# Kernel optimization log

Hardware: AMD Instinct MI355X
Metric: run time of the kernel (lower is better)

Reference implementation:

```python
import jax, jax.numpy as jnp
import numpy as np

B = 8192; N_LEAF = 34; N_SUB = 11; D0 = 32; ES = 64; EA = 128; H = 4
ETH = slice(0, 8); IP = slice(8, 19); TCP = slice(19, 34)
TCPF = slice(0, 8); IPF = slice(8, 11)


def setup_inputs() -> dict:
    key = jax.random.key(0)
    ks = jax.random.split(key, 32)
    w = lambda i, s: jax.random.normal(ks[i], s, dtype=jnp.float32) * 0.05
    return {
        "leaf_feats": jax.random.normal(ks[0], (B, N_LEAF, D0), dtype=jnp.float32),
        "sub_feats": jax.random.normal(ks[1], (B, N_SUB, D0), dtype=jnp.float32),
        "sub_align_W": w(2, (N_SUB, D0, ES)), "sub_align_b": w(3, (N_SUB, ES)),
        "leaf_align_W": w(4, (N_LEAF, D0, EA)), "leaf_align_b": w(5, (N_LEAF, EA)),
        "parent_align_W": w(6, (2, ES, EA)), "parent_align_b": w(7, (2, EA)),
        "sA_cls": w(8, (2, ES)), "sA_Wqkv": w(9, (2, 3 * ES, ES)), "sA_bqkv": w(10, (2, 3 * ES)),
        "sA_Wo": w(11, (2, ES, ES)), "sA_bo": w(12, (2, ES)),
        "sA_lng": jnp.ones((2, ES), jnp.float32), "sA_lnb": jnp.zeros((2, ES), jnp.float32),
        "sA_W1": w(13, (2, ES, 4 * ES)), "sA_b1": w(14, (2, 4 * ES)),
        "sA_W2": w(15, (2, 4 * ES, ES)), "sA_b2": w(16, (2, ES)),
        "pA_cls": w(17, (4, EA)), "pA_Wqkv": w(18, (4, 3 * EA, EA)), "pA_bqkv": w(19, (4, 3 * EA)),
        "pA_Wo": w(20, (4, EA, EA)), "pA_bo": w(21, (4, EA)),
        "pA_lng": jnp.ones((4, EA), jnp.float32), "pA_lnb": jnp.zeros((4, EA), jnp.float32),
        "pA_W1": w(22, (4, EA, 4 * EA)), "pA_b1": w(23, (4, 4 * EA)),
        "pA_W2": w(24, (4, 4 * EA, EA)), "pA_b2": w(25, (4, EA)),
        "clf_W": w(26, (EA, 2)), "clf_b": w(27, (2,)),
    }


def _ln(t, g, b):
    m = jnp.mean(t, -1, keepdims=True)
    v = jnp.var(t, -1, keepdims=True)
    return (t - m) / jnp.sqrt(v + 1e-5) * g + b


def _agg(x, cls, Wqkv, bqkv, Wo, bo, lng, lnb, W1, b1, W2, b2):
    # AttentionAggregator: prepend CLS, MHA, shared LayerNorm twice, FFN; return CLS output.
    Bx, _, E = x.shape
    d = E // H
    xc = jnp.concatenate([jnp.broadcast_to(cls, (Bx, 1, E)), x], axis=1)  # [B,S,E]
    S = xc.shape[1]
    qkv = xc @ Wqkv.T + bqkv                      # torch MHA in_proj layout [3E,E]
    q, k, v = jnp.split(qkv, 3, axis=-1)
    sh = lambda t: t.reshape(Bx, S, H, d).transpose(0, 2, 1, 3)
    q, k, v = sh(q), sh(k), sh(v)
    a = jax.nn.softmax(jnp.einsum('bhqd,bhkd->bhqk', q, k) * (1.0 / np.sqrt(d)), axis=-1)
    o = jnp.einsum('bhqk,bhkd->bhqd', a, v).transpose(0, 2, 1, 3).reshape(Bx, S, E)
    o = o @ Wo.T + bo
    h = _ln(xc + o, lng, lnb)
    f = jax.nn.gelu(h @ W1 + b1, approximate=False) @ W2 + b2
    h = _ln(h + f, lng, lnb)
    return h[:, 0]


def reference(leaf_feats, sub_feats, sub_align_W, sub_align_b, leaf_align_W, leaf_align_b,
              parent_align_W, parent_align_b,
              sA_cls, sA_Wqkv, sA_bqkv, sA_Wo, sA_bo, sA_lng, sA_lnb, sA_W1, sA_b1, sA_W2, sA_b2,
              pA_cls, pA_Wqkv, pA_bqkv, pA_Wo, pA_bo, pA_lng, pA_lnb, pA_W1, pA_b1, pA_W2, pA_b2,
              clf_W, clf_b):
    sA = lambda i: (sA_cls[i], sA_Wqkv[i], sA_bqkv[i], sA_Wo[i], sA_bo[i], sA_lng[i], sA_lnb[i],
                    sA_W1[i], sA_b1[i], sA_W2[i], sA_b2[i])
    pA = lambda i: (pA_cls[i], pA_Wqkv[i], pA_bqkv[i], pA_Wo[i], pA_bo[i], pA_lng[i], pA_lnb[i],
                    pA_W1[i], pA_b1[i], pA_W2[i], pA_b2[i])
    # subfield align (per-subfield Linear, batched) + aggregate
    sub_al = jnp.einsum('bsd,sde->bse', sub_feats, sub_align_W) + sub_align_b  # [B,11,64]
    tcpf = _agg(sub_al[:, TCPF], *sA(0))   # tcp.flags -> [B,64]
    ipf = _agg(sub_al[:, IPF], *sA(1))     # ip.flags  -> [B,64]
    # per-field aligners to aligned_dim=128
    leaf_al = jnp.einsum('bfd,fde->bfe', leaf_feats, leaf_align_W) + leaf_align_b  # [B,34,128]
    parent_al = jnp.stack([tcpf @ parent_align_W[0] + parent_align_b[0],
                           ipf @ parent_align_W[1] + parent_align_b[1]], axis=1)   # [B,2,128]
    eth_vec = _agg(leaf_al[:, ETH], *pA(0))
    ip_vec = _agg(jnp.concatenate([leaf_al[:, IP], parent_al[:, 1:2]], axis=1), *pA(1))
    tcp_vec = _agg(jnp.concatenate([leaf_al[:, TCP], parent_al[:, 0:1]], axis=1), *pA(2))
    pkt = _agg(jnp.stack([eth_vec, ip_vec, tcp_vec], axis=1), *pA(3))
    return pkt @ clf_W + clf_b
```

## Files before the change

kernel.cpp:

```cpp
#include <hip/hip_runtime.h>
#include <math.h>

#define G 4
#define NT 256


enum {
  I_LEAF = 0, I_SUB, I_SAW, I_SAB, I_LAW, I_LAB, I_PAW, I_PAB,
  I_SCLS, I_SWQKV, I_SBQKV, I_SWO, I_SBO, I_SLNG, I_SLNB, I_SW1, I_SB1, I_SW2, I_SB2,
  I_PCLS, I_PWQKV, I_PBQKV, I_PWO, I_PBO, I_PLNG, I_PLNB, I_PW1, I_PB1, I_PW2, I_PB2,
  I_CLFW, I_CLFB
};

struct P {
  const float* in[32];
  float* parent_al;
  float* vecs;
  float* out;
};

__device__ float g_usb[6][520];

__device__ __align__(16) float g_svT[2][64 * 64];
__device__ __align__(16) float g_soT[2][64 * 64];
__device__ __align__(16) float g_pvT[4][128 * 128];
__device__ __align__(16) float g_poT[4][128 * 128];

__device__ __forceinline__ void LD8(const float* p, float* o) {
  float4 a = ((const float4*)p)[0], b = ((const float4*)p)[1];
  o[0] = a.x; o[1] = a.y; o[2] = a.z; o[3] = a.w;
  o[4] = b.x; o[5] = b.y; o[6] = b.z; o[7] = b.w;
}
__device__ __forceinline__ void fma8(float& acc, const float* x, const float* w) {
#pragma unroll
  for (int i = 0; i < 8; ++i) acc += x[i] * w[i];
}
__device__ __forceinline__ float gelu(float v) {
  return 0.5f * v * (1.0f + erff(v * 0.70710678118654752f));
}

template <int E>
__device__ void ln_rows(float* buf, const float* __restrict__ gg, const float* __restrict__ bb) {
  const int w = threadIdx.x >> 6, lane = threadIdx.x & 63;
  for (int g = w; g < G; g += 4) {
    float* row = buf + g * E;
    float s = 0.f, s2 = 0.f;
    for (int e = lane; e < E; e += 64) { float x = row[e]; s += x; s2 += x * x; }
#pragma unroll
    for (int off = 1; off < 64; off <<= 1) {
      s += __shfl_xor(s, off, 64);
      s2 += __shfl_xor(s2, off, 64);
    }
    float m = s / (float)E;
    float inv = 1.0f / sqrtf(s2 / (float)E - m * m + 1e-5f);
    for (int e = lane; e < E; e += 64) row[e] = (row[e] - m) * inv * gg[e] + bb[e];
  }
}

__global__ __launch_bounds__(NT) void k_setup(P p) {
  const int a = blockIdx.x;
  const int tid = threadIdx.x;
  __shared__ float clsb[128];
  __shared__ float qb[128];
  int E;
  const float *Wq, *bq, *cls;
  if (a < 2) {
    E = 64;
    Wq = p.in[I_SWQKV] + (size_t)a * 192 * 64;
    bq = p.in[I_SBQKV] + a * 192;
    cls = p.in[I_SCLS] + a * 64;
  } else {
    E = 128;
    int i = a - 2;
    Wq = p.in[I_PWQKV] + (size_t)i * 384 * 128;
    bq = p.in[I_PBQKV] + i * 384;
    cls = p.in[I_PCLS] + i * 128;
  }
  const int D = E / 4;
  const float scale = (E == 64) ? 0.25f : 0.17677669529663687f;
  if (tid < E) clsb[tid] = cls[tid];
  __syncthreads();
  if (tid < E) {
    float acc = bq[tid];
    const float* w = Wq + (size_t)tid * E;
    for (int k = 0; k < E; k += 8) {
      float wv[8];
      LD8(w + k, wv);
#pragma unroll
      for (int ii = 0; ii < 8; ++ii) acc += clsb[k + ii] * wv[ii];
    }
    qb[tid] = acc;
  }
  __syncthreads();
  if (tid < E) {
    for (int h = 0; h < 4; ++h) {
      float acc = 0.f;
      for (int d = 0; d < D; ++d)
        acc += Wq[(size_t)(E + h * D + d) * E + tid] * qb[h * D + d];
      g_usb[a][h * E + tid] = acc * scale;
    }
  }
  if (tid < 4) {
    float acc = 0.f;
    for (int d = 0; d < D; ++d) acc += qb[tid * D + d] * bq[E + tid * D + d];
    g_usb[a][4 * E + tid] = acc * scale;
  }
  if (a < 2) {
    const float* Wv = p.in[I_SWQKV] + (size_t)a * 192 * 64 + 2 * 64 * 64;
    const float* Wo = p.in[I_SWO] + (size_t)a * 64 * 64;
    for (int idx = tid; idx < 64 * 64; idx += NT) {
      int k = idx >> 6, e = idx & 63;
      g_svT[a][idx] = Wv[(size_t)e * 64 + k];
      g_soT[a][idx] = Wo[(size_t)e * 64 + k];
    }
  } else {
    int i = a - 2;
    const float* Wv = p.in[I_PWQKV] + (size_t)i * 384 * 128 + 2 * 128 * 128;
    const float* Wo = p.in[I_PWO] + (size_t)i * 128 * 128;
    for (int idx = tid; idx < 128 * 128; idx += NT) {
      int k = idx >> 7, e = idx & 127;
      g_pvT[i][idx] = Wv[(size_t)e * 128 + k];
      g_poT[i][idx] = Wo[(size_t)e * 128 + k];
    }
  }
}

template <int E, int T, int XP>
__device__ void agg_run(const float* X, const float* clsb,
                        const float* uL, const float* sbL,
                        const float* __restrict__ WvT, const float* __restrict__ bv,
                        const float* __restrict__ WoT, const float* __restrict__ bo,
                        const float* __restrict__ lng, const float* __restrict__ lnb,
                        const float* __restrict__ W1, const float* __restrict__ b1,
                        const float* __restrict__ W2, const float* __restrict__ b2,
                        float* att, float* xbar, float* ob, float* hb, float* mid,
                        float* partial) {
  const int tid = threadIdx.x;
  constexpr int S = T + 1, KS = NT / E, KCH = E / KS;
  constexpr int M1 = (4 * E) / NT, KCH2 = (4 * E) / KS;

  for (int i = tid; i < G * 4 * S; i += NT) {
    int s = i % S, hh = (i / S) % 4, g = i / (4 * S);
    const float* u = uL + hh * XP;
    const float* x = (s == 0) ? clsb : (X + (size_t)(g * T + s - 1) * XP);
    float acc = sbL[hh];
    for (int k = 0; k < E; k += 8) {
      float xv[8], uv[8];
      LD8(x + k, xv);
      LD8(u + k, uv);
      fma8(acc, xv, uv);
    }
    att[(g * 4 + hh) * S + s] = acc;
  }
  __syncthreads();
  for (int i = tid; i < G * 4; i += NT) {
    float* a = att + i * S;
    float mx = a[0];
    for (int s = 1; s < S; ++s) mx = fmaxf(mx, a[s]);
    float sum = 0.f;
    for (int s = 0; s < S; ++s) { float e = expf(a[s] - mx); a[s] = e; sum += e; }
    float inv = 1.0f / sum;
    for (int s = 0; s < S; ++s) a[s] *= inv;
  }
  __syncthreads();
  constexpr int NI = (G * 4 * E) / NT;
  float xacc[NI];
#pragma unroll
  for (int n = 0; n < NI; ++n) {
    int i = tid + n * NT;
    int k = i % E, hh = (i / E) % 4, g = i / (4 * E);
    const float* a = att + (g * 4 + hh) * S;
    float acc = a[0] * clsb[k];
    for (int s = 1; s < S; ++s) acc += a[s] * X[(size_t)(g * T + s - 1) * XP + k];
    xacc[n] = acc;
  }
  __syncthreads();
#pragma unroll
  for (int n = 0; n < NI; ++n) xbar[tid + n * NT] = xacc[n];
  __syncthreads();
  {
    const int e = tid % E, ks = tid / E, hh = e / (E / 4);
    float acc[G];
#pragma unroll
    for (int g = 0; g < G; ++g) acc[g] = 0.f;
    for (int kc = 0; kc < KCH; kc += 8) {
      float wv[8];
#pragma unroll
      for (int ii = 0; ii < 8; ++ii)
        wv[ii] = WvT[(size_t)(ks * KCH + kc + ii) * E + e];
#pragma unroll
      for (int g = 0; g < G; ++g) {
        float xv[8];
        LD8(xbar + (g * 4 + hh) * E + ks * KCH + kc, xv);
        fma8(acc[g], xv, wv);
      }
    }
#pragma unroll
    for (int g = 0; g < G; ++g) partial[(ks * G + g) * E + e] = acc[g];
  }
  __syncthreads();
  for (int i = tid; i < G * E; i += NT) {
    int e = i % E, g = i / E;
    float v = bv[e];
#pragma unroll
    for (int ks = 0; ks < KS; ++ks) v += partial[(ks * G + g) * E + e];
    ob[g * E + e] = v;
  }
  __syncthreads();
  {
    const int e = tid % E, ks = tid / E;
    float acc[G];
#pragma unroll
    for (int g = 0; g < G; ++g) acc[g] = 0.f;
    for (int kc = 0; kc < KCH; kc += 8) {
      float wv[8];
#pragma unroll
      for (int ii = 0; ii < 8; ++ii)
        wv[ii] = WoT[(size_t)(ks * KCH + kc + ii) * E + e];
#pragma unroll
      for (int g = 0; g < G; ++g) {
        float xv[8];
        LD8(ob + g * E + ks * KCH + kc, xv);
        fma8(acc[g], xv, wv);
      }
    }
#pragma unroll
    for (int g = 0; g < G; ++g) partial[(ks * G + g) * E + e] = acc[g];
  }
  __syncthreads();
  for (int i = tid; i < G * E; i += NT) {
    int e = i % E, g = i / E;
    float v = bo[e] + clsb[e];
#pragma unroll
    for (int ks = 0; ks < KS; ++ks) v += partial[(ks * G + g) * E + e];
    hb[g * E + e] = v;
  }
  __syncthreads();
  ln_rows<E>(hb, lng, lnb);
  __syncthreads();
  {
    float acc[M1][G];
#pragma unroll
    for (int r = 0; r < M1; ++r)
#pragma unroll
      for (int g = 0; g < G; ++g) acc[r][g] = 0.f;
    for (int j = 0; j < E; j += 8) {
      float wv[M1][8];
#pragma unroll
      for (int ii = 0; ii < 8; ++ii) {
        if constexpr (M1 == 2) {
          float2 w2 = *(const float2*)(W1 + (size_t)(j + ii) * 4 * E + 2 * tid);
          wv[0][ii] = w2.x;
          wv[1][ii] = w2.y;
        } else {
          wv[0][ii] = W1[(size_t)(j + ii) * 4 * E + tid];
        }
      }
#pragma unroll
      for (int g = 0; g < G; ++g) {
        float xv[8];
        LD8(hb + g * E + j, xv);
#pragma unroll
        for (int r = 0; r < M1; ++r) fma8(acc[r][g], xv, wv[r]);
      }
    }
#pragma unroll
    for (int r = 0; r < M1; ++r) {
      int m = tid * M1 + r;
      float bias = b1[m];
#pragma unroll
      for (int g = 0; g < G; ++g) mid[g * 4 * E + m] = gelu(acc[r][g] + bias);
    }
  }
  __syncthreads();
  {
    const int e = tid % E, ks = tid / E, m0 = ks * KCH2;
    float acc[G];
#pragma unroll
    for (int g = 0; g < G; ++g) acc[g] = 0.f;
    for (int mc = 0; mc < KCH2; mc += 8) {
      float wv[8];
#pragma unroll
      for (int ii = 0; ii < 8; ++ii) wv[ii] = W2[(size_t)(m0 + mc + ii) * E + e];
#pragma unroll
      for (int g = 0; g < G; ++g) {
        float xv[8];
        LD8(mid + g * 4 * E + m0 + mc, xv);
        fma8(acc[g], xv, wv);
      }
    }
#pragma unroll
    for (int g = 0; g < G; ++g) partial[(ks * G + g) * E + e] = acc[g];
  }
  __syncthreads();
  for (int i = tid; i < G * E; i += NT) {
    int e = i % E, g = i / E;
    float v = b2[e] + hb[g * E + e];
#pragma unroll
    for (int ks = 0; ks < KS; ++ks) v += partial[(ks * G + g) * E + e];
    ob[g * E + e] = v;
  }
  __syncthreads();
  ln_rows<E>(ob, lng, lnb);
  __syncthreads();
}

template <int T, int F0, int AI>
__device__ void sub_body(const P& p, int b0) {
  constexpr int XP = 68;
  const int tid = threadIdx.x;
  __shared__ __align__(16) float X[G * T * XP];
  __shared__ __align__(16) float clsb[64];
  __shared__ __align__(16) float uL[4 * XP];
  __shared__ __align__(16) float sbL[4];
  __shared__ __align__(16) float att[G * 4 * (T + 1)];
  __shared__ __align__(16) float xbar[G * 4 * 64];
  __shared__ __align__(16) float ob[G * 64];
  __shared__ __align__(16) float hb[G * 64];
  __shared__ __align__(16) float mid[G * 256];
  __shared__ __align__(16) float partial[4 * G * 64];

  const float* subf = p.in[I_SUB];
  const float* saW = p.in[I_SAW];
  const float* sab = p.in[I_SAB];
  for (int i = tid; i < T * 64; i += NT) {
    int f = i / 64, e = i % 64;
    float bias = sab[(F0 + f) * 64 + e];
    float acc[G];
#pragma unroll
    for (int g = 0; g < G; ++g) acc[g] = bias;
    for (int d = 0; d < 32; d += 8) {
      float wv[8];
#pragma unroll
      for (int ii = 0; ii < 8; ++ii)
        wv[ii] = saW[(size_t)((F0 + f) * 32 + d + ii) * 64 + e];
#pragma unroll
      for (int g = 0; g < G; ++g) {
        float xv[8];
        LD8(subf + (size_t)(b0 + g) * 352 + (F0 + f) * 32 + d, xv);
        fma8(acc[g], xv, wv);
      }
    }
#pragma unroll
    for (int g = 0; g < G; ++g) X[(g * T + f) * XP + e] = acc[g];
  }
  for (int i = tid; i < 4 * 64; i += NT) uL[(i >> 6) * XP + (i & 63)] = g_usb[AI][i];
  if (tid < 4) sbL[tid] = g_usb[AI][256 + tid];
  if (tid < 64) clsb[tid] = p.in[I_SCLS][AI * 64 + tid];
  __syncthreads();

  agg_run<64, T, XP>(X, clsb, uL, sbL,
                     g_svT[AI], p.in[I_SBQKV] + AI * 192 + 128,
                     g_soT[AI], p.in[I_SBO] + AI * 64,
                     p.in[I_SLNG] + AI * 64, p.in[I_SLNB] + AI * 64,
                     p.in[I_SW1] + AI * 64 * 256, p.in[I_SB1] + AI * 256,
                     p.in[I_SW2] + AI * 256 * 64, p.in[I_SB2] + AI * 64,
                     att, xbar, ob, hb, mid, partial);
  for (int i = tid; i < G * 64; i += NT) {
    int e = i % 64, g = i / 64;
    p.vecs[(size_t)(b0 + g) * 384 + AI * 64 + e] = ob[g * 64 + e];
  }
}

__global__ __launch_bounds__(NT, 4) void k_sub_agg0(P p) { sub_body<8, 0, 0>(p, blockIdx.x * G); }
__global__ __launch_bounds__(NT, 4) void k_sub_agg1(P p) { sub_body<3, 8, 1>(p, blockIdx.x * G); }

__global__ __launch_bounds__(NT, 4) void k_pal(P p) {
  __shared__ __align__(16) float tf[G * 128];
  const int tid = threadIdx.x, b0 = blockIdx.x * G;
  for (int i = tid; i < G * 128; i += NT) {
    int g = i / 128, r = i % 128;
    tf[i] = p.vecs[(size_t)(b0 + g) * 384 + r];
  }
  __syncthreads();
  const int pi = tid >> 7, e = tid & 127;
  const float* paW = p.in[I_PAW];
  float bias = p.in[I_PAB][pi * 128 + e];
  float acc[G];
#pragma unroll
  for (int g = 0; g < G; ++g) acc[g] = bias;
  for (int j = 0; j < 64; j += 8) {
    float wv[8];
#pragma unroll
    for (int ii = 0; ii < 8; ++ii) wv[ii] = paW[(size_t)(pi * 64 + j + ii) * 128 + e];
#pragma unroll
    for (int g = 0; g < G; ++g) {
      float xv[8];
      LD8(tf + g * 128 + pi * 64 + j, xv);
      fma8(acc[g], xv, wv);
    }
  }
#pragma unroll
  for (int g = 0; g < G; ++g)
    p.parent_al[(size_t)(b0 + g) * 256 + pi * 128 + e] = acc[g];
}

#define PXP 132
#define OVL 6144

template <int T, int F, int F0, int PAR, int AI>
__device__ void parent_body(const P& p, int b0, float* arena, float* clsb,
                            float* uL, float* sbL, float* att) {
  const int tid = threadIdx.x;
  float* X = arena;
  const float* leaf = p.in[I_LEAF];
  const float* laW = p.in[I_LAW];
  const float* lab = p.in[I_LAB];
  for (int i = tid; i < F * 128; i += NT) {
    int f = i / 128, e = i % 128;
    float bias = lab[(F0 + f) * 128 + e];
    float acc[G];
#pragma unroll
    for (int g = 0; g < G; ++g) acc[g] = bias;
    for (int d = 0; d < 32; d += 8) {
      float wv[8];
#pragma unroll
      for (int ii = 0; ii < 8; ++ii)
        wv[ii] = laW[(size_t)((F0 + f) * 32 + d + ii) * 128 + e];
#pragma unroll
      for (int g = 0; g < G; ++g) {
        float xv[8];
        LD8(leaf + (size_t)(b0 + g) * 1088 + (F0 + f) * 32 + d, xv);
        fma8(acc[g], xv, wv);
      }
    }
#pragma unroll
    for (int g = 0; g < G; ++g) X[(g * T + f) * PXP + e] = acc[g];
  }
  if constexpr (PAR >= 0) {
    for (int i = tid; i < G * 128; i += NT) {
      int g = i / 128, e = i % 128;
      X[(g * T + T - 1) * PXP + e] = p.parent_al[(size_t)(b0 + g) * 256 + PAR * 128 + e];
    }
  }
  for (int i = tid; i < 4 * 128; i += NT) uL[(i >> 7) * PXP + (i & 127)] = g_usb[2 + AI][i];
  if (tid < 4) sbL[tid] = g_usb[2 + AI][512 + tid];
  if (tid < 128) clsb[tid] = p.in[I_PCLS][AI * 128 + tid];
  __syncthreads();

  float* xbar = arena;
  float* partial = arena + 2048;
  float* ob = arena + 3072;
  float* hb = arena + 3584;
  float* mid = arena + 4096;
  agg_run<128, T, PXP>(X, clsb, uL, sbL,
                       g_pvT[AI], p.in[I_PBQKV] + AI * 384 + 256,
                       g_poT[AI], p.in[I_PBO] + AI * 128,
                       p.in[I_PLNG] + AI * 128, p.in[I_PLNB] + AI * 128,
                       p.in[I_PW1] + (size_t)AI * 128 * 512, p.in[I_PB1] + AI * 512,
                       p.in[I_PW2] + (size_t)AI * 512 * 128, p.in[I_PB2] + AI * 128,
                       att, xbar, ob, hb, mid, partial);
  for (int i = tid; i < G * 128; i += NT) {
    int e = i % 128, g = i / 128;
    p.vecs[(size_t)(b0 + g) * 384 + AI * 128 + e] = ob[g * 128 + e];
  }
}

#define PARENT_KERNEL(NAME, T, F, F0, PAR, AI, ASZ)                         \
__global__ __launch_bounds__(NT, 4) void NAME(P p) {                        \
  __shared__ __align__(16) float arena[ASZ];                                \
  __shared__ __align__(16) float clsb[128];                                 \
  __shared__ __align__(16) float uL[4 * PXP];                               \
  __shared__ __align__(16) float sbL[4];                                    \
  __shared__ __align__(16) float att[G * 4 * (T + 1)];                      \
  parent_body<T, F, F0, PAR, AI>(p, blockIdx.x * G, arena, clsb, uL, sbL, att); \
}

PARENT_KERNEL(k_parent0,  8,  8,  0, -1, 0, OVL)
PARENT_KERNEL(k_parent1, 12, 11,  8,  1, 1, G * 12 * PXP)
PARENT_KERNEL(k_parent2, 16, 15, 19,  0, 2, G * 16 * PXP)

__global__ __launch_bounds__(NT, 4) void k_pkt(P p) {
  __shared__ __align__(16) float arena[OVL];
  __shared__ __align__(16) float clsb[128];
  __shared__ __align__(16) float uL[4 * PXP];
  __shared__ __align__(16) float sbL[4];
  __shared__ __align__(16) float att[G * 4 * 4];
  const int tid = threadIdx.x, b0 = blockIdx.x * G;
  float* X = arena;

  for (int i = tid; i < 3 * G * 128; i += NT) {
    int e = i % 128, g = (i / 128) % G, t = i / (G * 128);
    X[(g * 3 + t) * PXP + e] = p.vecs[(size_t)(b0 + g) * 384 + t * 128 + e];
  }
  for (int i = tid; i < 4 * 128; i += NT) uL[(i >> 7) * PXP + (i & 127)] = g_usb[5][i];
  if (tid < 4) sbL[tid] = g_usb[5][512 + tid];
  if (tid < 128) clsb[tid] = p.in[I_PCLS][3 * 128 + tid];
  __syncthreads();

  float* xbar = arena;
  float* partial = arena + 2048;
  float* ob = arena + 3072;
  float* hb = arena + 3584;
  float* mid = arena + 4096;
  agg_run<128, 3, PXP>(X, clsb, uL, sbL,
                       g_pvT[3], p.in[I_PBQKV] + 3 * 384 + 256,
                       g_poT[3], p.in[I_PBO] + 3 * 128,
                       p.in[I_PLNG] + 3 * 128, p.in[I_PLNB] + 3 * 128,
                       p.in[I_PW1] + (size_t)3 * 128 * 512, p.in[I_PB1] + 3 * 512,
                       p.in[I_PW2] + (size_t)3 * 512 * 128, p.in[I_PB2] + 3 * 128,
                       att, xbar, ob, hb, mid, partial);

  if (tid < G * 2) {
    int g = tid >> 1, c = tid & 1;
    const float* cw = p.in[I_CLFW];
    float acc = p.in[I_CLFB][c];
    for (int j = 0; j < 128; ++j) acc += ob[g * 128 + j] * cw[j * 2 + c];
    p.out[(size_t)(b0 + g) * 2 + c] = acc;
  }
}

extern "C" void kernel_launch(void* const* d_in, const int* in_sizes, int n_in,
                              void* d_out, int out_size, void* d_ws, size_t ws_size,
                              hipStream_t stream) {
  P p;
  for (int i = 0; i < 32; ++i) p.in[i] = (const float*)d_in[i];
  const int B = in_sizes[0] / (34 * 32);
  float* ws = (float*)d_ws;
  p.parent_al = ws;
  p.vecs = ws + (size_t)B * 256;
  p.out = (float*)d_out;

  k_setup<<<dim3(6), dim3(NT), 0, stream>>>(p);
  k_sub_agg0<<<dim3(B / G), dim3(NT), 0, stream>>>(p);
  k_sub_agg1<<<dim3(B / G), dim3(NT), 0, stream>>>(p);
  k_pal<<<dim3(B / G), dim3(NT), 0, stream>>>(p);
  k_parent0<<<dim3(B / G), dim3(NT), 0, stream>>>(p);
  k_parent1<<<dim3(B / G), dim3(NT), 0, stream>>>(p);
  k_parent2<<<dim3(B / G), dim3(NT), 0, stream>>>(p);
  k_pkt<<<dim3(B / G), dim3(NT), 0, stream>>>(p);
}
```

Before: 943.1 us.

## Split each aggregator kernel into separate attention and FFN kernels

Each attention aggregator kernel is split in two. The first computes attention plus the first LayerNorm and writes the intermediate to global workspace. The second reloads it and runs the FFN and second LayerNorm. The aim is to shrink per-kernel shared memory and register footprint so more blocks fit per CU. The cost is six more kernel launches plus an extra global write and read of the intermediate vectors, and the FFN kernels may become weight-bandwidth bound.

```diff
diff --git a/kernel.cpp b/kernel.cpp
--- a/kernel.cpp
+++ b/kernel.cpp
@@ -126,18 +126,15 @@
 }
 
 template <int E, int T, int XP>
-__device__ void agg_run(const float* X, const float* clsb,
-                        const float* uL, const float* sbL,
-                        const float* __restrict__ WvT, const float* __restrict__ bv,
-                        const float* __restrict__ WoT, const float* __restrict__ bo,
-                        const float* __restrict__ lng, const float* __restrict__ lnb,
-                        const float* __restrict__ W1, const float* __restrict__ b1,
-                        const float* __restrict__ W2, const float* __restrict__ b2,
-                        float* att, float* xbar, float* ob, float* hb, float* mid,
-                        float* partial) {
+__device__ void agg_attn(const float* X, const float* clsb,
+                         const float* uL, const float* sbL,
+                         const float* __restrict__ WvT, const float* __restrict__ bv,
+                         const float* __restrict__ WoT, const float* __restrict__ bo,
+                         const float* __restrict__ lng, const float* __restrict__ lnb,
+                         float* att, float* xbar, float* ob, float* hb,
+                         float* partial) {
   const int tid = threadIdx.x;
   constexpr int S = T + 1, KS = NT / E, KCH = E / KS;
-  constexpr int M1 = (4 * E) / NT, KCH2 = (4 * E) / KS;
 
   for (int i = tid; i < G * 4 * S; i += NT) {
     int s = i % S, hh = (i / S) % 4, g = i / (4 * S);
@@ -238,6 +235,15 @@
   __syncthreads();
   ln_rows<E>(hb, lng, lnb);
   __syncthreads();
+}
+
+template <int E>
+__device__ void agg_ffn(const float* __restrict__ W1, const float* __restrict__ b1,
+                        const float* __restrict__ W2, const float* __restrict__ b2,
+                        const float* __restrict__ lng, const float* __restrict__ lnb,
+                        float* hb, float* mid, float* partial, float* ob) {
+  const int tid = threadIdx.x;
+  constexpr int KS = NT / E, M1 = (4 * E) / NT, KCH2 = (4 * E) / KS;
   {
     float acc[M1][G];
 #pragma unroll
@@ -305,20 +311,16 @@
   __syncthreads();
 }
 
-template <int T, int F0, int AI>
-__device__ void sub_body(const P& p, int b0) {
+template <int T, int F0, int AI, int ASZ>
+__device__ void sub_attn_body(const P& p, int b0) {
   constexpr int XP = 68;
   const int tid = threadIdx.x;
-  __shared__ __align__(16) float X[G * T * XP];
+  __shared__ __align__(16) float arena[ASZ];
   __shared__ __align__(16) float clsb[64];
   __shared__ __align__(16) float uL[4 * XP];
   __shared__ __align__(16) float sbL[4];
   __shared__ __align__(16) float att[G * 4 * (T + 1)];
-  __shared__ __align__(16) float xbar[G * 4 * 64];
-  __shared__ __align__(16) float ob[G * 64];
-  __shared__ __align__(16) float hb[G * 64];
-  __shared__ __align__(16) float mid[G * 256];
-  __shared__ __align__(16) float partial[4 * G * 64];
+  float* X = arena;
 
   const float* subf = p.in[I_SUB];
   const float* saW = p.in[I_SAW];
@@ -349,21 +351,47 @@
   if (tid < 64) clsb[tid] = p.in[I_SCLS][AI * 64 + tid];
   __syncthreads();
 
-  agg_run<64, T, XP>(X, clsb, uL, sbL,
-                     g_svT[AI], p.in[I_SBQKV] + AI * 192 + 128,
-                     g_soT[AI], p.in[I_SBO] + AI * 64,
-                     p.in[I_SLNG] + AI * 64, p.in[I_SLNB] + AI * 64,
-                     p.in[I_SW1] + AI * 64 * 256, p.in[I_SB1] + AI * 256,
-                     p.in[I_SW2] + AI * 256 * 64, p.in[I_SB2] + AI * 64,
-                     att, xbar, ob, hb, mid, partial);
+  float* xbar = arena;
+  float* partial = arena + 1024;
+  float* ob = arena + 2048;
+  float* hb = arena + 2304;
+  agg_attn<64, T, XP>(X, clsb, uL, sbL,
+                      g_svT[AI], p.in[I_SBQKV] + AI * 192 + 128,
+                      g_soT[AI], p.in[I_SBO] + AI * 64,
+                      p.in[I_SLNG] + AI * 64, p.in[I_SLNB] + AI * 64,
+                      att, xbar, ob, hb, partial);
+  for (int i = tid; i < G * 64; i += NT) {
+    int e = i % 64, g = i / 64;
+    p.vecs[(size_t)(b0 + g) * 384 + AI * 64 + e] = hb[g * 64 + e];
+  }
+}
+
+__global__ __launch_bounds__(NT, 4) void k_sattn0(P p) { sub_attn_body<8, 0, 0, 2560>(p, blockIdx.x * G); }
+__global__ __launch_bounds__(NT, 4) void k_sattn1(P p) { sub_attn_body<3, 8, 1, 2560>(p, blockIdx.x * G); }
+
+template <int AI>
+__device__ void sub_ffn_body(const P& p, int b0) {
+  const int tid = threadIdx.x;
+  __shared__ __align__(16) float hb[G * 64];
+  __shared__ __align__(16) float mid[G * 256];
+  __shared__ __align__(16) float partial[4 * G * 64];
+  __shared__ __align__(16) float ob[G * 64];
+  for (int i = tid; i < G * 64; i += NT) {
+    int e = i % 64, g = i / 64;
+    hb[i] = p.vecs[(size_t)(b0 + g) * 384 + AI * 64 + e];
+  }
+  __syncthreads();
+  agg_ffn<64>(p.in[I_SW1] + AI * 64 * 256, p.in[I_SB1] + AI * 256,
+              p.in[I_SW2] + AI * 256 * 64, p.in[I_SB2] + AI * 64,
+              p.in[I_SLNG] + AI * 64, p.in[I_SLNB] + AI * 64,
+              hb, mid, partial, ob);
   for (int i = tid; i < G * 64; i += NT) {
     int e = i % 64, g = i / 64;
     p.vecs[(size_t)(b0 + g) * 384 + AI * 64 + e] = ob[g * 64 + e];
   }
 }
-
-__global__ __launch_bounds__(NT, 4) void k_sub_agg0(P p) { sub_body<8, 0, 0>(p, blockIdx.x * G); }
-__global__ __launch_bounds__(NT, 4) void k_sub_agg1(P p) { sub_body<3, 8, 1>(p, blockIdx.x * G); }
+__global__ __launch_bounds__(NT, 4) void k_sffn0(P p) { sub_ffn_body<0>(p, blockIdx.x * G); }
+__global__ __launch_bounds__(NT, 4) void k_sffn1(P p) { sub_ffn_body<1>(p, blockIdx.x * G); }
 
 __global__ __launch_bounds__(NT, 4) void k_pal(P p) {
   __shared__ __align__(16) float tf[G * 128];
@@ -396,11 +424,10 @@
 }
 
 #define PXP 132
-#define OVL 6144
 
 template <int T, int F, int F0, int PAR, int AI>
-__device__ void parent_body(const P& p, int b0, float* arena, float* clsb,
-                            float* uL, float* sbL, float* att) {
+__device__ void pattn_body(const P& p, int b0, float* arena, float* clsb,
+                           float* uL, float* sbL, float* att) {
   const int tid = threadIdx.x;
   float* X = arena;
   const float* leaf = p.in[I_LEAF];
@@ -442,36 +469,58 @@
   float* partial = arena + 2048;
   float* ob = arena + 3072;
   float* hb = arena + 3584;
-  float* mid = arena + 4096;
-  agg_run<128, T, PXP>(X, clsb, uL, sbL,
-                       g_pvT[AI], p.in[I_PBQKV] + AI * 384 + 256,
-                       g_poT[AI], p.in[I_PBO] + AI * 128,
-                       p.in[I_PLNG] + AI * 128, p.in[I_PLNB] + AI * 128,
-                       p.in[I_PW1] + (size_t)AI * 128 * 512, p.in[I_PB1] + AI * 512,
-                       p.in[I_PW2] + (size_t)AI * 512 * 128, p.in[I_PB2] + AI * 128,
-                       att, xbar, ob, hb, mid, partial);
+  agg_attn<128, T, PXP>(X, clsb, uL, sbL,
+                        g_pvT[AI], p.in[I_PBQKV] + AI * 384 + 256,
+                        g_poT[AI], p.in[I_PBO] + AI * 128,
+                        p.in[I_PLNG] + AI * 128, p.in[I_PLNB] + AI * 128,
+                        att, xbar, ob, hb, partial);
   for (int i = tid; i < G * 128; i += NT) {
     int e = i % 128, g = i / 128;
-    p.vecs[(size_t)(b0 + g) * 384 + AI * 128 + e] = ob[g * 128 + e];
-  }
-}
-
-#define PARENT_KERNEL(NAME, T, F, F0, PAR, AI, ASZ)                         \
+    p.vecs[(size_t)(b0 + g) * 384 + AI * 128 + e] = hb[g * 128 + e];
+  }
+}
+
+#define PATTN_KERNEL(NAME, T, F, F0, PAR, AI, ASZ)                          \
 __global__ __launch_bounds__(NT, 4) void NAME(P p) {                        \
   __shared__ __align__(16) float arena[ASZ];                                \
   __shared__ __align__(16) float clsb[128];                                 \
   __shared__ __align__(16) float uL[4 * PXP];                               \
   __shared__ __align__(16) float sbL[4];                                    \
   __shared__ __align__(16) float att[G * 4 * (T + 1)];                      \
-  parent_body<T, F, F0, PAR, AI>(p, blockIdx.x * G, arena, clsb, uL, sbL, att); \
-}
-
-PARENT_KERNEL(k_parent0,  8,  8,  0, -1, 0, OVL)
-PARENT_KERNEL(k_parent1, 12, 11,  8,  1, 1, G * 12 * PXP)
-PARENT_KERNEL(k_parent2, 16, 15, 19,  0, 2, G * 16 * PXP)
-
-__global__ __launch_bounds__(NT, 4) void k_pkt(P p) {
-  __shared__ __align__(16) float arena[OVL];
+  pattn_body<T, F, F0, PAR, AI>(p, blockIdx.x * G, arena, clsb, uL, sbL, att); \
+}
+
+PATTN_KERNEL(k_pattn0,  8,  8,  0, -1, 0, G * 8 * PXP)
+PATTN_KERNEL(k_pattn1, 12, 11,  8,  1, 1, G * 12 * PXP)
+PATTN_KERNEL(k_pattn2, 16, 15, 19,  0, 2, G * 16 * PXP)
+
+template <int AI>
+__device__ void pffn_body(const P& p, int b0) {
+  const int tid = threadIdx.x;
+  __shared__ __align__(16) float hb[G * 128];
+  __shared__ __align__(16) float mid[G * 512];
+  __shared__ __align__(16) float partial[2 * G * 128];
+  __shared__ __align__(16) float ob[G * 128];
+  for (int i = tid; i < G * 128; i += NT) {
+    int e = i % 128, g = i / 128;
+    hb[i] = p.vecs[(size_t)(b0 + g) * 384 + AI * 128 + e];
+  }
+  __syncthreads();
+  agg_ffn<128>(p.in[I_PW1] + (size_t)AI * 128 * 512, p.in[I_PB1] + AI * 512,
+               p.in[I_PW2] + (size_t)AI * 512 * 128, p.in[I_PB2] + AI * 128,
+               p.in[I_PLNG] + AI * 128, p.in[I_PLNB] + AI * 128,
+               hb, mid, partial, ob);
+  for (int i = tid; i < G * 128; i += NT) {
+    int e = i % 128, g = i / 128;
+    p.vecs[(size_t)(b0 + g) * 384 + AI * 128 + e] = ob[g * 128 + e];
+  }
+}
+__global__ __launch_bounds__(NT, 4) void k_pffn0(P p) { pffn_body<0>(p, blockIdx.x * G); }
+__global__ __launch_bounds__(NT, 4) void k_pffn1(P p) { pffn_body<1>(p, blockIdx.x * G); }
+__global__ __launch_bounds__(NT, 4) void k_pffn2(P p) { pffn_body<2>(p, blockIdx.x * G); }
+
+__global__ __launch_bounds__(NT, 4) void k_pkt_attn(P p) {
+  __shared__ __align__(16) float arena[4096];
   __shared__ __align__(16) float clsb[128];
   __shared__ __align__(16) float uL[4 * PXP];
   __shared__ __align__(16) float sbL[4];
@@ -492,15 +541,32 @@
   float* partial = arena + 2048;
   float* ob = arena + 3072;
   float* hb = arena + 3584;
-  float* mid = arena + 4096;
-  agg_run<128, 3, PXP>(X, clsb, uL, sbL,
-                       g_pvT[3], p.in[I_PBQKV] + 3 * 384 + 256,
-                       g_poT[3], p.in[I_PBO] + 3 * 128,
-                       p.in[I_PLNG] + 3 * 128, p.in[I_PLNB] + 3 * 128,
-                       p.in[I_PW1] + (size_t)3 * 128 * 512, p.in[I_PB1] + 3 * 512,
-                       p.in[I_PW2] + (size_t)3 * 512 * 128, p.in[I_PB2] + 3 * 128,
-                       att, xbar, ob, hb, mid, partial);
-
+  agg_attn<128, 3, PXP>(X, clsb, uL, sbL,
+                        g_pvT[3], p.in[I_PBQKV] + 3 * 384 + 256,
+                        g_poT[3], p.in[I_PBO] + 3 * 128,
+                        p.in[I_PLNG] + 3 * 128, p.in[I_PLNB] + 3 * 128,
+                        att, xbar, ob, hb, partial);
+  for (int i = tid; i < G * 128; i += NT) {
+    int e = i % 128, g = i / 128;
+    p.parent_al[(size_t)(b0 + g) * 256 + e] = hb[g * 128 + e];
+  }
+}
+
+__global__ __launch_bounds__(NT, 4) void k_pkt_ffn(P p) {
+  const int tid = threadIdx.x, b0 = blockIdx.x * G;
+  __shared__ __align__(16) float hb[G * 128];
+  __shared__ __align__(16) float mid[G * 512];
+  __shared__ __align__(16) float partial[2 * G * 128];
+  __shared__ __align__(16) float ob[G * 128];
+  for (int i = tid; i < G * 128; i += NT) {
+    int e = i % 128, g = i / 128;
+    hb[i] = p.parent_al[(size_t)(b0 + g) * 256 + e];
+  }
+  __syncthreads();
+  agg_ffn<128>(p.in[I_PW1] + (size_t)3 * 128 * 512, p.in[I_PB1] + 3 * 512,
+               p.in[I_PW2] + (size_t)3 * 512 * 128, p.in[I_PB2] + 3 * 128,
+               p.in[I_PLNG] + 3 * 128, p.in[I_PLNB] + 3 * 128,
+               hb, mid, partial, ob);
   if (tid < G * 2) {
     int g = tid >> 1, c = tid & 1;
     const float* cw = p.in[I_CLFW];
@@ -520,13 +586,20 @@
   p.parent_al = ws;
   p.vecs = ws + (size_t)B * 256;
   p.out = (float*)d_out;
-
-  k_setup<<<dim3(6), dim3(NT), 0, stream>>>(p);
-  k_sub_agg0<<<dim3(B / G), dim3(NT), 0, stream>>>(p);
-  k_sub_agg1<<<dim3(B / G), dim3(NT), 0, stream>>>(p);
-  k_pal<<<dim3(B / G), dim3(NT), 0, stream>>>(p);
-  k_parent0<<<dim3(B / G), dim3(NT), 0, stream>>>(p);
-  k_parent1<<<dim3(B / G), dim3(NT), 0, stream>>>(p);
-  k_parent2<<<dim3(B / G), dim3(NT), 0, stream>>>(p);
-  k_pkt<<<dim3(B / G), dim3(NT), 0, stream>>>(p);
-}
+  const dim3 grid(B / G), blk(NT);
+
+  k_setup<<<dim3(6), blk, 0, stream>>>(p);
+  k_sattn0<<<grid, blk, 0, stream>>>(p);
+  k_sffn0<<<grid, blk, 0, stream>>>(p);
+  k_sattn1<<<grid, blk, 0, stream>>>(p);
+  k_sffn1<<<grid, blk, 0, stream>>>(p);
+  k_pal<<<grid, blk, 0, stream>>>(p);
+  k_pattn0<<<grid, blk, 0, stream>>>(p);
+  k_pffn0<<<grid, blk, 0, stream>>>(p);
+  k_pattn1<<<grid, blk, 0, stream>>>(p);
+  k_pffn1<<<grid, blk, 0, stream>>>(p);
+  k_pattn2<<<grid, blk, 0, stream>>>(p);
+  k_pffn2<<<grid, blk, 0, stream>>>(p);
+  k_pkt_attn<<<grid, blk, 0, stream>>>(p);
+  k_pkt_ffn<<<grid, blk, 0, stream>>>(p);
+}
```

New measurement: 1.056 ms. 1.12x slower.

## Merge independent aggregators into one launch, fuse parent align, parallelize softmax

Applied to the files above, without the earlier changes.

The two subfield aggregators and the eth parent aggregator, which have no mutual dependency, now run in a single kernel split by blockIdx.y over a shared-memory arena. The parent-align projection is folded into the ip/tcp parent kernels, removing the separate k_pal launch and its global round trip. The eth result is stored in the freed parent_al buffer. Softmax now uses 16 lanes per row with wave shuffles instead of one thread per row. Together these cut launches and let independent work fill the GPU, at the cost of a redundant parent-align computation and a larger shared-memory footprint for the merged kernel.

```diff
diff --git a/kernel.cpp b/kernel.cpp
--- a/kernel.cpp
+++ b/kernel.cpp
@@ -153,14 +153,22 @@
     att[(g * 4 + hh) * S + s] = acc;
   }
   __syncthreads();
-  for (int i = tid; i < G * 4; i += NT) {
-    float* a = att + i * S;
-    float mx = a[0];
-    for (int s = 1; s < S; ++s) mx = fmaxf(mx, a[s]);
-    float sum = 0.f;
-    for (int s = 0; s < S; ++s) { float e = expf(a[s] - mx); a[s] = e; sum += e; }
+  {
+    const int grp = tid >> 4, l = tid & 15;
+    float* a = att + grp * S;
+    float v0 = (l < S) ? a[l] : -3.0e38f;
+    float v1 = (l + 16 < S) ? a[l + 16] : -3.0e38f;
+    float mx = fmaxf(v0, v1);
+#pragma unroll
+    for (int off = 1; off < 16; off <<= 1) mx = fmaxf(mx, __shfl_xor(mx, off, 64));
+    float e0 = (l < S) ? expf(v0 - mx) : 0.f;
+    float e1 = (l + 16 < S) ? expf(v1 - mx) : 0.f;
+    float sum = e0 + e1;
+#pragma unroll
+    for (int off = 1; off < 16; off <<= 1) sum += __shfl_xor(sum, off, 64);
     float inv = 1.0f / sum;
-    for (int s = 0; s < S; ++s) a[s] *= inv;
+    if (l < S) a[l] = e0 * inv;
+    if (l + 16 < S) a[l + 16] = e1 * inv;
   }
   __syncthreads();
   constexpr int NI = (G * 4 * E) / NT;
@@ -305,21 +313,14 @@
   __syncthreads();
 }
 
+#define PXP 132
+
 template <int T, int F0, int AI>
-__device__ void sub_body(const P& p, int b0) {
+__device__ void sub_body(const P& p, int b0, float* arena, float* clsb,
+                         float* uL, float* sbL, float* att) {
   constexpr int XP = 68;
   const int tid = threadIdx.x;
-  __shared__ __align__(16) float X[G * T * XP];
-  __shared__ __align__(16) float clsb[64];
-  __shared__ __align__(16) float uL[4 * XP];
-  __shared__ __align__(16) float sbL[4];
-  __shared__ __align__(16) float att[G * 4 * (T + 1)];
-  __shared__ __align__(16) float xbar[G * 4 * 64];
-  __shared__ __align__(16) float ob[G * 64];
-  __shared__ __align__(16) float hb[G * 64];
-  __shared__ __align__(16) float mid[G * 256];
-  __shared__ __align__(16) float partial[4 * G * 64];
-
+  float* X = arena;
   const float* subf = p.in[I_SUB];
   const float* saW = p.in[I_SAW];
   const float* sab = p.in[I_SAB];
@@ -349,6 +350,11 @@
   if (tid < 64) clsb[tid] = p.in[I_SCLS][AI * 64 + tid];
   __syncthreads();
 
+  float* xbar = arena;
+  float* partial = arena + 1024;
+  float* ob = arena + 2048;
+  float* hb = arena + 2304;
+  float* mid = arena + 2560;
   agg_run<64, T, XP>(X, clsb, uL, sbL,
                      g_svT[AI], p.in[I_SBQKV] + AI * 192 + 128,
                      g_soT[AI], p.in[I_SBO] + AI * 64,
@@ -362,50 +368,18 @@
   }
 }
 
-__global__ __launch_bounds__(NT, 4) void k_sub_agg0(P p) { sub_body<8, 0, 0>(p, blockIdx.x * G); }
-__global__ __launch_bounds__(NT, 4) void k_sub_agg1(P p) { sub_body<3, 8, 1>(p, blockIdx.x * G); }
-
-__global__ __launch_bounds__(NT, 4) void k_pal(P p) {
-  __shared__ __align__(16) float tf[G * 128];
-  const int tid = threadIdx.x, b0 = blockIdx.x * G;
-  for (int i = tid; i < G * 128; i += NT) {
-    int g = i / 128, r = i % 128;
-    tf[i] = p.vecs[(size_t)(b0 + g) * 384 + r];
-  }
-  __syncthreads();
-  const int pi = tid >> 7, e = tid & 127;
-  const float* paW = p.in[I_PAW];
-  float bias = p.in[I_PAB][pi * 128 + e];
-  float acc[G];
-#pragma unroll
-  for (int g = 0; g < G; ++g) acc[g] = bias;
-  for (int j = 0; j < 64; j += 8) {
-    float wv[8];
-#pragma unroll
-    for (int ii = 0; ii < 8; ++ii) wv[ii] = paW[(size_t)(pi * 64 + j + ii) * 128 + e];
-#pragma unroll
-    for (int g = 0; g < G; ++g) {
-      float xv[8];
-      LD8(tf + g * 128 + pi * 64 + j, xv);
-      fma8(acc[g], xv, wv);
-    }
-  }
-#pragma unroll
-  for (int g = 0; g < G; ++g)
-    p.parent_al[(size_t)(b0 + g) * 256 + pi * 128 + e] = acc[g];
-}
-
-#define PXP 132
-#define OVL 6144
-
-template <int T, int F, int F0, int PAR, int AI>
+template <int T, int F, int F0, int PI, int AI>
 __device__ void parent_body(const P& p, int b0, float* arena, float* clsb,
-                            float* uL, float* sbL, float* att) {
+                            float* uL, float* sbL, float* att, float* tf) {
   const int tid = threadIdx.x;
   float* X = arena;
   const float* leaf = p.in[I_LEAF];
   const float* laW = p.in[I_LAW];
   const float* lab = p.in[I_LAB];
+  if constexpr (PI >= 0) {
+    for (int i = tid; i < G * 64; i += NT)
+      tf[i] = p.vecs[(size_t)(b0 + i / 64) * 384 + PI * 64 + (i & 63)];
+  }
   for (int i = tid; i < F * 128; i += NT) {
     int f = i / 128, e = i % 128;
     float bias = lab[(F0 + f) * 128 + e];
@@ -427,10 +401,22 @@
 #pragma unroll
     for (int g = 0; g < G; ++g) X[(g * T + f) * PXP + e] = acc[g];
   }
-  if constexpr (PAR >= 0) {
+  if constexpr (PI >= 0) {
+    __syncthreads();
+    const float* paW = p.in[I_PAW] + (size_t)PI * 64 * 128;
+    const float* pab = p.in[I_PAB] + PI * 128;
     for (int i = tid; i < G * 128; i += NT) {
       int g = i / 128, e = i % 128;
-      X[(g * T + T - 1) * PXP + e] = p.parent_al[(size_t)(b0 + g) * 256 + PAR * 128 + e];
+      float acc = pab[e];
+      const float* f = tf + g * 64;
+      for (int j = 0; j < 64; j += 8) {
+        float wv[8], fv[8];
+        LD8(f + j, fv);
+#pragma unroll
+        for (int ii = 0; ii < 8; ++ii) wv[ii] = paW[(size_t)(j + ii) * 128 + e];
+        fma8(acc, fv, wv);
+      }
+      X[(g * T + T - 1) * PXP + e] = acc;
     }
   }
   for (int i = tid; i < 4 * 128; i += NT) uL[(i >> 7) * PXP + (i & 127)] = g_usb[2 + AI][i];
@@ -452,26 +438,49 @@
                        att, xbar, ob, hb, mid, partial);
   for (int i = tid; i < G * 128; i += NT) {
     int e = i % 128, g = i / 128;
-    p.vecs[(size_t)(b0 + g) * 384 + AI * 128 + e] = ob[g * 128 + e];
-  }
-}
-
-#define PARENT_KERNEL(NAME, T, F, F0, PAR, AI, ASZ)                         \
-__global__ __launch_bounds__(NT, 4) void NAME(P p) {                        \
-  __shared__ __align__(16) float arena[ASZ];                                \
-  __shared__ __align__(16) float clsb[128];                                 \
-  __shared__ __align__(16) float uL[4 * PXP];                               \
-  __shared__ __align__(16) float sbL[4];                                    \
-  __shared__ __align__(16) float att[G * 4 * (T + 1)];                      \
-  parent_body<T, F, F0, PAR, AI>(p, blockIdx.x * G, arena, clsb, uL, sbL, att); \
-}
-
-PARENT_KERNEL(k_parent0,  8,  8,  0, -1, 0, OVL)
-PARENT_KERNEL(k_parent1, 12, 11,  8,  1, 1, G * 12 * PXP)
-PARENT_KERNEL(k_parent2, 16, 15, 19,  0, 2, G * 16 * PXP)
+    if constexpr (AI == 0)
+      p.parent_al[(size_t)(b0 + g) * 256 + e] = ob[g * 128 + e];
+    else
+      p.vecs[(size_t)(b0 + g) * 384 + AI * 128 + e] = ob[g * 128 + e];
+  }
+}
+
+__global__ __launch_bounds__(NT, 4) void k_lvl1(P p) {
+  __shared__ __align__(16) float arena[6144];
+  __shared__ __align__(16) float clsb[128];
+  __shared__ __align__(16) float uL[4 * PXP];
+  __shared__ __align__(16) float sbL[4];
+  __shared__ __align__(16) float att[G * 4 * 9];
+  const int b0 = blockIdx.x * G;
+  if (blockIdx.y == 0)
+    sub_body<8, 0, 0>(p, b0, arena, clsb, uL, sbL, att);
+  else if (blockIdx.y == 1)
+    sub_body<3, 8, 1>(p, b0, arena, clsb, uL, sbL, att);
+  else
+    parent_body<8, 8, 0, -1, 0>(p, b0, arena, clsb, uL, sbL, att, nullptr);
+}
+
+__global__ __launch_bounds__(NT, 4) void k_parent1(P p) {
+  __shared__ __align__(16) float arena[G * 12 * PXP];
+  __shared__ __align__(16) float clsb[128];
+  __shared__ __align__(16) float uL[4 * PXP];
+  __shared__ __align__(16) float sbL[4];
+  __shared__ __align__(16) float att[G * 4 * 13];
+  __shared__ __align__(16) float tf[G * 64];
+  parent_body<12, 11, 8, 1, 1>(p, blockIdx.x * G, arena, clsb, uL, sbL, att, tf);
+}
+__global__ __launch_bounds__(NT, 4) void k_parent2(P p) {
+  __shared__ __align__(16) float arena[G * 16 * PXP];
+  __shared__ __align__(16) float clsb[128];
+  __shared__ __align__(16) float uL[4 * PXP];
+  __shared__ __align__(16) float sbL[4];
+  __shared__ __align__(16) float att[G * 4 * 17];
+  __shared__ __align__(16) float tf[G * 64];
+  parent_body<16, 15, 19, 0, 2>(p, blockIdx.x * G, arena, clsb, uL, sbL, att, tf);
+}
 
 __global__ __launch_bounds__(NT, 4) void k_pkt(P p) {
-  __shared__ __align__(16) float arena[OVL];
+  __shared__ __align__(16) float arena[6144];
   __shared__ __align__(16) float clsb[128];
   __shared__ __align__(16) float uL[4 * PXP];
   __shared__ __align__(16) float sbL[4];
@@ -481,7 +490,9 @@
 
   for (int i = tid; i < 3 * G * 128; i += NT) {
     int e = i % 128, g = (i / 128) % G, t = i / (G * 128);
-    X[(g * 3 + t) * PXP + e] = p.vecs[(size_t)(b0 + g) * 384 + t * 128 + e];
+    float v = (t == 0) ? p.parent_al[(size_t)(b0 + g) * 256 + e]
+                       : p.vecs[(size_t)(b0 + g) * 384 + t * 128 + e];
+    X[(g * 3 + t) * PXP + e] = v;
   }
   for (int i = tid; i < 4 * 128; i += NT) uL[(i >> 7) * PXP + (i & 127)] = g_usb[5][i];
   if (tid < 4) sbL[tid] = g_usb[5][512 + tid];
@@ -520,13 +531,11 @@
   p.parent_al = ws;
   p.vecs = ws + (size_t)B * 256;
   p.out = (float*)d_out;
-
-  k_setup<<<dim3(6), dim3(NT), 0, stream>>>(p);
-  k_sub_agg0<<<dim3(B / G), dim3(NT), 0, stream>>>(p);
-  k_sub_agg1<<<dim3(B / G), dim3(NT), 0, stream>>>(p);
-  k_pal<<<dim3(B / G), dim3(NT), 0, stream>>>(p);
-  k_parent0<<<dim3(B / G), dim3(NT), 0, stream>>>(p);
-  k_parent1<<<dim3(B / G), dim3(NT), 0, stream>>>(p);
-  k_parent2<<<dim3(B / G), dim3(NT), 0, stream>>>(p);
-  k_pkt<<<dim3(B / G), dim3(NT), 0, stream>>>(p);
-}
+  const dim3 blk(NT);
+
+  k_setup<<<dim3(6), blk, 0, stream>>>(p);
+  k_lvl1<<<dim3(B / G, 3), blk, 0, stream>>>(p);
+  k_parent1<<<dim3(B / G), blk, 0, stream>>>(p);
+  k_parent2<<<dim3(B / G), blk, 0, stream>>>(p);
+  k_pkt<<<dim3(B / G), blk, 0, stream>>>(p);
+}
```

Measured after the change: 984.9 us. 4.4% more time.
